# Kernel tuning notes

Measured on AMD Instinct MI355X. Metric: run time of the kernel, lower is better.

Reference implementation:

```python
import jax, jax.numpy as jnp
import numpy as np

N, D, H, E = 50000, 128, 128, 800000


def setup_inputs() -> dict:
    key = jax.random.key(0)
    ks = jax.random.split(key, 12)
    p = lambda k, shape: jax.random.normal(k, shape, dtype=jnp.float32) * 0.02
    z = lambda n: jnp.zeros((n,), jnp.float32)
    return {
        "x1": jax.random.normal(ks[0], (N, D), dtype=jnp.float32),
        "edge_index1": jax.random.randint(ks[1], (2, E), 0, N, dtype=jnp.int32),
        "x2": jax.random.normal(ks[2], (N, D), dtype=jnp.float32),
        "edge_index2": jax.random.randint(ks[3], (2, E), 0, N, dtype=jnp.int32),
        "enc_w1": p(ks[4], (D, H)), "enc_b1": z(H),
        "enc_w2": p(ks[5], (H, H)), "enc_b2": z(H),
        "conv1_w": p(ks[6], (H, H)), "conv1_b": z(H),
        "conv2_w": p(ks[7], (H, H)), "conv2_b": z(H),
        "sim_w1": p(ks[8], (4 * H, H)), "sim_b1": z(H),
        "sim_w2": p(ks[9], (H, 1)), "sim_b2": z(1),
    }


def reference(x1, edge_index1, x2, edge_index2,
              enc_w1, enc_b1, enc_w2, enc_b2,
              conv1_w, conv1_b, conv2_w, conv2_b,
              sim_w1, sim_b1, sim_w2, sim_b2):
    def gcn(x, ei, W, b):
        row, col = ei[0], ei[1]            # [E], [E]
        h = x @ W + b                      # [N, H]
        n = x.shape[0]
        deg = jax.ops.segment_sum(jnp.ones(row.shape[0], h.dtype), row, num_segments=n)
        dis = jnp.where(deg > 0, deg ** -0.5, 0.0)   # deg^-0.5, inf -> 0
        norm = dis[row] * dis[col]         # [E]
        msg = h[col] * norm[:, None]       # gather + per-edge scale, [E, H]
        return jax.ops.segment_sum(msg, row, num_segments=n)  # scatter-add

    def embed(x, ei):
        h = jax.nn.relu(x @ enc_w1 + enc_b1) @ enc_w2 + enc_b2  # encoder MLP
        h = jax.nn.relu(gcn(h, ei, conv1_w, conv1_b))
        h = jax.nn.relu(gcn(h, ei, conv2_w, conv2_b))
        return h.mean(axis=0)              # mean pooling -> [H]

    g1 = embed(x1, edge_index1)
    g2 = embed(x2, edge_index2)
    c = jnp.concatenate([g1, g2, jnp.abs(g1 - g2), g1 * g2], axis=-1)  # [4H]
    return jax.nn.relu(c @ sim_w1 + sim_b1) @ sim_w2 + sim_b2          # [1]
```

## Files before the change

kernel.cpp:

```cpp
#include <hip/hip_runtime.h>
#include <hip/hip_bf16.h>

#define HD 128

typedef short bf16x8 __attribute__((ext_vector_type(8)));
typedef float f32x4 __attribute__((ext_vector_type(4)));

static __device__ inline unsigned short f2b(float f) {
  __hip_bfloat16 h = __float2bfloat16(f);
  return *(unsigned short*)&h;
}
static __device__ inline float b2f(unsigned short u) {
  return __uint_as_float(((unsigned int)u) << 16);
}
static __device__ inline float unpack_lo(unsigned int v) {
  return __uint_as_float(v << 16);
}
static __device__ inline float unpack_hi(unsigned int v) {
  return __uint_as_float(v & 0xffff0000u);
}
static __device__ inline unsigned int pack2(float lo, float hi) {
  return (unsigned int)f2b(lo) | ((unsigned int)f2b(hi) << 16);
}

__global__ void k_deg_slot(const int* __restrict__ ei0, const int* __restrict__ ei1,
                           int E, int N, int* __restrict__ deg2, int* __restrict__ slot) {
  int g = blockIdx.y;
  const int* rows = (g ? ei1 : ei0);
  int base = (blockIdx.x * 256 + threadIdx.x) * 8;
  int* deg = deg2 + g * N;
  int* sl = slot + g * E;
  if (base + 7 < E) {
    int4 r0 = *(const int4*)(rows + base);
    int4 r1 = *(const int4*)(rows + base + 4);
    int4 s0, s1;
    s0.x = atomicAdd(&deg[r0.x], 1);
    s0.y = atomicAdd(&deg[r0.y], 1);
    s0.z = atomicAdd(&deg[r0.z], 1);
    s0.w = atomicAdd(&deg[r0.w], 1);
    s1.x = atomicAdd(&deg[r1.x], 1);
    s1.y = atomicAdd(&deg[r1.y], 1);
    s1.z = atomicAdd(&deg[r1.z], 1);
    s1.w = atomicAdd(&deg[r1.w], 1);
    *(int4*)(sl + base) = s0;
    *(int4*)(sl + base + 4) = s1;
  } else {
    for (int e = base; e < E; ++e) sl[e] = atomicAdd(&deg[rows[e]], 1);
  }
}

__global__ void k_scan_block(const int* __restrict__ deg, int* __restrict__ offs,
                             int* __restrict__ partials, int Ntot) {
  __shared__ int s[256];
  int t = threadIdx.x;
  int i = blockIdx.x * 256 + t;
  int v = (i < Ntot) ? deg[i] : 0;
  s[t] = v;
  __syncthreads();
  #pragma unroll
  for (int off = 1; off < 256; off <<= 1) {
    int x = (t >= off) ? s[t - off] : 0;
    __syncthreads();
    s[t] += x;
    __syncthreads();
  }
  if (i < Ntot) offs[i] = s[t] - v;
  if (t == 255) partials[blockIdx.x] = s[255];
}

__global__ void k_scan_partials(int* __restrict__ partials, int P) {
  __shared__ int s[512];
  int t = threadIdx.x;
  int v = (t < P) ? partials[t] : 0;
  s[t] = v;
  __syncthreads();
  #pragma unroll
  for (int off = 1; off < 512; off <<= 1) {
    int x = (t >= off) ? s[t - off] : 0;
    __syncthreads();
    s[t] += x;
    __syncthreads();
  }
  if (t < P) partials[t] = s[t] - v;
}

__global__ void k_scan_finalize(int* __restrict__ offs, const int* __restrict__ partials,
                                const int* __restrict__ deg, float* __restrict__ dis,
                                int Ntot, int Etot) {
  int i = blockIdx.x * 256 + threadIdx.x;
  if (i < Ntot) {
    offs[i] += partials[blockIdx.x];
    int d = deg[i];
    dis[i] = (d > 0) ? (1.0f / sqrtf((float)d)) : 0.0f;
  }
  if (blockIdx.x == 0 && threadIdx.x == 0) offs[Ntot] = Etot;
}

__global__ void k_csr_fill(const int* __restrict__ ei0, const int* __restrict__ ei1,
                           int E, int N, const int* __restrict__ offs,
                           const int* __restrict__ slot, unsigned short* __restrict__ csr_col) {
  int g = blockIdx.y;
  const int* eg = (g ? ei1 : ei0);
  const int* ob = offs + g * N;
  const int* sl = slot + g * E;
  int base = (blockIdx.x * 256 + threadIdx.x) * 4;
  if (base + 3 < E) {
    int4 r = *(const int4*)(eg + base);
    int4 c = *(const int4*)(eg + E + base);
    int4 s = *(const int4*)(sl + base);
    csr_col[ob[r.x] + s.x] = (unsigned short)c.x;
    csr_col[ob[r.y] + s.y] = (unsigned short)c.y;
    csr_col[ob[r.z] + s.z] = (unsigned short)c.z;
    csr_col[ob[r.w] + s.w] = (unsigned short)c.w;
  } else {
    for (int e = base; e < E; ++e)
      csr_col[ob[eg[e]] + sl[e]] = (unsigned short)eg[E + e];
  }
}

__global__ void k_cvt_w(const float* __restrict__ w0, const float* __restrict__ w1,
                        const float* __restrict__ w2, const float* __restrict__ w3,
                        unsigned short* __restrict__ Wf) {
  int m = blockIdx.x >> 6;
  const float* W = (m == 0) ? w0 : (m == 1) ? w1 : (m == 2) ? w2 : w3;
  int idx = (blockIdx.x & 63) * 256 + threadIdx.x;
  int n = idx & 127, k = idx >> 7;
  float w = W[(size_t)k * HD + n];
  unsigned short h = f2b(w);
  unsigned short l = f2b(w - b2f(h));
  int nt = n >> 4, n16 = n & 15, kc = k >> 5, q = (k >> 3) & 3, j = k & 7;
  int lanei = 16 * q + n16;
  size_t off = ((size_t)(nt * 4 + kc) * 64 + lanei) * 8 + j;
  unsigned short* base = Wf + (size_t)m * 32768;
  base[off] = h;
  base[16384 + off] = l;
}

template<bool RELU, bool SCALE, bool CVT>
__global__ __launch_bounds__(256, 2) void k_gemm_lds(
    const unsigned short* __restrict__ Ab,
    const float* __restrict__ Af0, const float* __restrict__ Af1,
    const unsigned short* __restrict__ Wf, const float* __restrict__ bias,
    const float* __restrict__ scale, unsigned short* __restrict__ C,
    int N, int Ntot) {
  __shared__ unsigned short lds[32768];
  const int tid = threadIdx.x;
  #pragma unroll
  for (int i = 0; i < 16; ++i)
    *(float4*)&lds[(size_t)(i * 256 + tid) * 8] = *(const float4*)&Wf[(size_t)(i * 256 + tid) * 8];
  __syncthreads();

  const int lane = tid & 63;
  const int wave = tid >> 6;
  const int n16 = lane & 15, q = lane >> 4;
  const int rowbase = blockIdx.x * 256 + wave * 64;

  int arow[4];
  #pragma unroll
  for (int t = 0; t < 4; ++t) {
    int r = rowbase + 16 * t + n16;
    arow[t] = (r < Ntot) ? r : (Ntot - 1);
  }

  f32x4 acc[4][8];
  #pragma unroll
  for (int t = 0; t < 4; ++t)
    #pragma unroll
    for (int nt = 0; nt < 8; ++nt) acc[t][nt] = (f32x4){0.f, 0.f, 0.f, 0.f};

  #pragma unroll
  for (int kc = 0; kc < 4; ++kc) {
    bf16x8 a[4];
    #pragma unroll
    for (int t = 0; t < 4; ++t) {
      if (CVT) {
        int r = arow[t];
        const float* src = (r < N) ? (Af0 + (size_t)r * HD) : (Af1 + (size_t)(r - N) * HD);
        float4 u0 = *(const float4*)(src + kc * 32 + q * 8);
        float4 u1 = *(const float4*)(src + kc * 32 + q * 8 + 4);
        union { unsigned short us[8]; bf16x8 v; } tmp;
        tmp.us[0] = f2b(u0.x); tmp.us[1] = f2b(u0.y);
        tmp.us[2] = f2b(u0.z); tmp.us[3] = f2b(u0.w);
        tmp.us[4] = f2b(u1.x); tmp.us[5] = f2b(u1.y);
        tmp.us[6] = f2b(u1.z); tmp.us[7] = f2b(u1.w);
        a[t] = tmp.v;
      } else {
        a[t] = *(const bf16x8*)(Ab + (size_t)arow[t] * HD + kc * 32 + q * 8);
      }
    }
    #pragma unroll
    for (int nt = 0; nt < 8; ++nt) {
      bf16x8 bh = *(const bf16x8*)&lds[(size_t)((nt * 4 + kc) * 64 + lane) * 8];
      bf16x8 bl = *(const bf16x8*)&lds[16384 + (size_t)((nt * 4 + kc) * 64 + lane) * 8];
      #pragma unroll
      for (int t = 0; t < 4; ++t) {
        acc[t][nt] = __builtin_amdgcn_mfma_f32_16x16x32_bf16(a[t], bh, acc[t][nt], 0, 0, 0);
        acc[t][nt] = __builtin_amdgcn_mfma_f32_16x16x32_bf16(a[t], bl, acc[t][nt], 0, 0, 0);
      }
    }
  }

  float bv[8];
  #pragma unroll
  for (int nt = 0; nt < 8; ++nt) bv[nt] = bias[nt * 16 + n16];

  #pragma unroll
  for (int t = 0; t < 4; ++t) {
    #pragma unroll
    for (int r = 0; r < 4; ++r) {
      int row = rowbase + 16 * t + 4 * q + r;
      if (row < Ntot) {
        float s = SCALE ? scale[row] : 1.0f;
        #pragma unroll
        for (int nt = 0; nt < 8; ++nt) {
          float v = acc[t][nt][r] + bv[nt];
          if (RELU) v = fmaxf(v, 0.f);
          if (SCALE) v *= s;
          C[(size_t)row * HD + nt * 16 + n16] = f2b(v);
        }
      }
    }
  }
}

template<bool POOL>
__global__ __launch_bounds__(256) void k_aggregate(
    const unsigned short* __restrict__ T, const int* __restrict__ offs,
    const unsigned short* __restrict__ csr_col, const float* __restrict__ dis,
    unsigned short* __restrict__ out, float* __restrict__ poolrep, int N, int Ntot) {
  __shared__ float red[4][128];
  const int lane = threadIdx.x & 63;
  const int wave = threadIdx.x >> 6;
  const int gw = blockIdx.x * 4 + wave;
  const int sub = lane >> 4, c16 = lane & 15;

  float ax[8];
  #pragma unroll
  for (int j = 0; j < 8; ++j) ax[j] = 0.f;

  if (gw < Ntot) {
    const int beg = offs[gw], end = offs[gw + 1];
    const unsigned int* Tg = (const unsigned int*)T + (size_t)(gw >= N ? N : 0) * 64;
    for (int e = beg; e < end; e += 16) {
      #pragma unroll
      for (int gp = 0; gp < 4; ++gp) {
        if (e + 4 * gp < end) {
          int eg = e + 4 * gp + sub;
          bool valid = (eg < end);
          int ce = valid ? eg : (end - 1);
          int col = csr_col[ce];
          uint4 v = *(const uint4*)(Tg + (size_t)col * 64 + c16 * 4);
          if (!valid) { v.x = 0; v.y = 0; v.z = 0; v.w = 0; }
          ax[0] += unpack_lo(v.x); ax[1] += unpack_hi(v.x);
          ax[2] += unpack_lo(v.y); ax[3] += unpack_hi(v.y);
          ax[4] += unpack_lo(v.z); ax[5] += unpack_hi(v.z);
          ax[6] += unpack_lo(v.w); ax[7] += unpack_hi(v.w);
        }
      }
    }
  }

  #pragma unroll
  for (int j = 0; j < 8; ++j) {
    ax[j] += __shfl_xor(ax[j], 32, 64);
    ax[j] += __shfl_xor(ax[j], 16, 64);
  }
  float dr = (gw < Ntot) ? dis[gw] : 0.f;
  #pragma unroll
  for (int j = 0; j < 8; ++j) ax[j] = fmaxf(ax[j] * dr, 0.f);

  if (!POOL) {
    if (gw < Ntot && sub == 0) {
      uint4 o;
      o.x = pack2(ax[0], ax[1]);
      o.y = pack2(ax[2], ax[3]);
      o.z = pack2(ax[4], ax[5]);
      o.w = pack2(ax[6], ax[7]);
      ((uint4*)out)[(size_t)gw * 16 + c16] = o;
    }
  } else {
    if (sub == 0) {
      *(float4*)&red[wave][c16 * 8]     = make_float4(ax[0], ax[1], ax[2], ax[3]);
      *(float4*)&red[wave][c16 * 8 + 4] = make_float4(ax[4], ax[5], ax[6], ax[7]);
    }
    __syncthreads();
    int t = threadIdx.x;
    if (t < 128) {
      float s = red[0][t] + red[1][t] + red[2][t] + red[3][t];
      int g = (blockIdx.x * 4 >= N) ? 1 : 0;
      atomicAdd(&poolrep[(size_t)((blockIdx.x & 15) * 2 + g) * 128 + t], s);
    }
  }
}

__global__ void k_final(const float* __restrict__ poolrep,
                        const float* __restrict__ W1, const float* __restrict__ b1,
                        const float* __restrict__ W2, const float* __restrict__ b2,
                        float* __restrict__ out, float invN) {
  __shared__ float cs[512];
  __shared__ float red[2];
  int t = threadIdx.x;
  float g1 = 0.f, g2 = 0.f;
  #pragma unroll
  for (int r = 0; r < 16; ++r) {
    g1 += poolrep[r * 256 + t];
    g2 += poolrep[r * 256 + 128 + t];
  }
  g1 *= invN;
  g2 *= invN;
  cs[t] = g1;
  cs[128 + t] = g2;
  cs[256 + t] = fabsf(g1 - g2);
  cs[384 + t] = g1 * g2;
  __syncthreads();
  float acc = b1[t];
  #pragma unroll 8
  for (int i = 0; i < 512; ++i) acc = fmaf(cs[i], W1[(size_t)i * HD + t], acc);
  float h = fmaxf(acc, 0.f);
  float v = h * W2[t];
  #pragma unroll
  for (int off = 32; off > 0; off >>= 1) v += __shfl_down(v, off, 64);
  if ((t & 63) == 0) red[t >> 6] = v;
  __syncthreads();
  if (t == 0) out[0] = red[0] + red[1] + b2[0];
}

extern "C" void kernel_launch(void* const* d_in, const int* in_sizes, int n_in,
                              void* d_out, int out_size, void* d_ws, size_t ws_size,
                              hipStream_t stream) {
  const float* x1     = (const float*)d_in[0];
  const int*   ei1    = (const int*)d_in[1];
  const float* x2     = (const float*)d_in[2];
  const int*   ei2    = (const int*)d_in[3];
  const float* W_in[4] = {(const float*)d_in[4], (const float*)d_in[6],
                          (const float*)d_in[8], (const float*)d_in[10]};
  const float* B_in[4] = {(const float*)d_in[5], (const float*)d_in[7],
                          (const float*)d_in[9], (const float*)d_in[11]};
  const float* sim_w1 = (const float*)d_in[12];
  const float* sim_b1 = (const float*)d_in[13];
  const float* sim_w2 = (const float*)d_in[14];
  const float* sim_b2 = (const float*)d_in[15];

  const int N = in_sizes[0] / HD;
  const int E = in_sizes[1] / 2;
  const int Ntot = 2 * N;

  unsigned short* sp = (unsigned short*)d_ws;
  unsigned short* bufA = sp; sp += (size_t)Ntot * HD;
  unsigned short* bufB = sp; sp += (size_t)Ntot * HD;
  unsigned short* Wf   = sp; sp += 4 * 32768;
  float* fp = (float*)sp;
  float* dis     = fp; fp += Ntot;
  float* poolrep = fp; fp += 16 * 256;
  int* ip = (int*)fp;
  int* deg2     = ip; ip += Ntot;
  int* offs     = ip; ip += Ntot + 1;
  int* partials = ip; ip += 512;
  ip += 1;
  int* slot     = ip; ip += 2 * E;
  unsigned short* csr_col = (unsigned short*)ip;

  const int scanBlocks = (Ntot + 255) / 256;
  const int gemmBlocks = (Ntot + 255) / 256;
  const int aggBlocks  = (Ntot + 3) / 4;
  const dim3 degGrid((E / 8 + 255) / 256, 2);
  const dim3 fillGrid((E / 4 + 255) / 256, 2);

  hipMemsetAsync(poolrep, 0, 16 * 256 * sizeof(float), stream);
  hipMemsetAsync(deg2, 0, (size_t)Ntot * sizeof(int), stream);

  k_cvt_w<<<256, 256, 0, stream>>>(W_in[0], W_in[1], W_in[2], W_in[3], Wf);

  k_deg_slot<<<degGrid, 256, 0, stream>>>(ei1, ei2, E, N, deg2, slot);
  k_scan_block<<<scanBlocks, 256, 0, stream>>>(deg2, offs, partials, Ntot);
  k_scan_partials<<<1, 512, 0, stream>>>(partials, scanBlocks);
  k_scan_finalize<<<scanBlocks, 256, 0, stream>>>(offs, partials, deg2, dis, Ntot, 2 * E);
  k_csr_fill<<<fillGrid, 256, 0, stream>>>(ei1, ei2, E, N, offs, slot, csr_col);

  k_gemm_lds<true,  false, true ><<<gemmBlocks, 256, 0, stream>>>(
      nullptr, x1, x2, Wf + 0 * 32768, B_in[0], nullptr, bufA, N, Ntot);
  k_gemm_lds<false, false, false><<<gemmBlocks, 256, 0, stream>>>(
      bufA, nullptr, nullptr, Wf + 1 * 32768, B_in[1], nullptr, bufB, N, Ntot);
  k_gemm_lds<false, true,  false><<<gemmBlocks, 256, 0, stream>>>(
      bufB, nullptr, nullptr, Wf + 2 * 32768, B_in[2], dis, bufA, N, Ntot);
  k_aggregate<false><<<aggBlocks, 256, 0, stream>>>(bufA, offs, csr_col, dis, bufB, nullptr, N, Ntot);
  k_gemm_lds<false, true,  false><<<gemmBlocks, 256, 0, stream>>>(
      bufB, nullptr, nullptr, Wf + 3 * 32768, B_in[3], dis, bufA, N, Ntot);
  k_aggregate<true ><<<aggBlocks, 256, 0, stream>>>(bufA, offs, csr_col, dis, nullptr, poolrep, N, Ntot);

  k_final<<<1, 128, 0, stream>>>(poolrep, sim_w1, sim_b1, sim_w2, sim_b2,
                                 (float*)d_out, 1.0f / (float)N);
}
```

Measured before the change: 452.3 us.

## Switch activations and weights to fp16 with packed fp16 aggregation

Result: faster. 423.5 us (-6.4%).

```diff
diff --git a/kernel.cpp b/kernel.cpp
--- a/kernel.cpp
+++ b/kernel.cpp
@@ -3,49 +3,34 @@
 
 #define HD 128
 
-typedef short bf16x8 __attribute__((ext_vector_type(8)));
+typedef _Float16 f16x8 __attribute__((ext_vector_type(8)));
+typedef _Float16 f16x2 __attribute__((ext_vector_type(2)));
 typedef float f32x4 __attribute__((ext_vector_type(4)));
 
-static __device__ inline unsigned short f2b(float f) {
-  __hip_bfloat16 h = __float2bfloat16(f);
-  return *(unsigned short*)&h;
-}
-static __device__ inline float b2f(unsigned short u) {
-  return __uint_as_float(((unsigned int)u) << 16);
-}
-static __device__ inline float unpack_lo(unsigned int v) {
-  return __uint_as_float(v << 16);
-}
-static __device__ inline float unpack_hi(unsigned int v) {
-  return __uint_as_float(v & 0xffff0000u);
-}
-static __device__ inline unsigned int pack2(float lo, float hi) {
-  return (unsigned int)f2b(lo) | ((unsigned int)f2b(hi) << 16);
-}
-
 __global__ void k_deg_slot(const int* __restrict__ ei0, const int* __restrict__ ei1,
-                           int E, int N, int* __restrict__ deg2, int* __restrict__ slot) {
+                           int E, int N, int* __restrict__ deg2,
+                           unsigned short* __restrict__ slot) {
   int g = blockIdx.y;
   const int* rows = (g ? ei1 : ei0);
   int base = (blockIdx.x * 256 + threadIdx.x) * 8;
   int* deg = deg2 + g * N;
-  int* sl = slot + g * E;
+  unsigned short* sl = slot + (size_t)g * E;
   if (base + 7 < E) {
     int4 r0 = *(const int4*)(rows + base);
     int4 r1 = *(const int4*)(rows + base + 4);
-    int4 s0, s1;
-    s0.x = atomicAdd(&deg[r0.x], 1);
-    s0.y = atomicAdd(&deg[r0.y], 1);
-    s0.z = atomicAdd(&deg[r0.z], 1);
-    s0.w = atomicAdd(&deg[r0.w], 1);
-    s1.x = atomicAdd(&deg[r1.x], 1);
-    s1.y = atomicAdd(&deg[r1.y], 1);
-    s1.z = atomicAdd(&deg[r1.z], 1);
-    s1.w = atomicAdd(&deg[r1.w], 1);
-    *(int4*)(sl + base) = s0;
-    *(int4*)(sl + base + 4) = s1;
+    union { unsigned short us[8]; uint4 v; } s;
+    s.us[0] = (unsigned short)atomicAdd(&deg[r0.x], 1);
+    s.us[1] = (unsigned short)atomicAdd(&deg[r0.y], 1);
+    s.us[2] = (unsigned short)atomicAdd(&deg[r0.z], 1);
+    s.us[3] = (unsigned short)atomicAdd(&deg[r0.w], 1);
+    s.us[4] = (unsigned short)atomicAdd(&deg[r1.x], 1);
+    s.us[5] = (unsigned short)atomicAdd(&deg[r1.y], 1);
+    s.us[6] = (unsigned short)atomicAdd(&deg[r1.z], 1);
+    s.us[7] = (unsigned short)atomicAdd(&deg[r1.w], 1);
+    *(uint4*)(sl + base) = s.v;
   } else {
-    for (int e = base; e < E; ++e) sl[e] = atomicAdd(&deg[rows[e]], 1);
+    for (int e = base; e < E; ++e)
+      sl[e] = (unsigned short)atomicAdd(&deg[rows[e]], 1);
   }
 }
 
@@ -98,20 +83,21 @@
 
 __global__ void k_csr_fill(const int* __restrict__ ei0, const int* __restrict__ ei1,
                            int E, int N, const int* __restrict__ offs,
-                           const int* __restrict__ slot, unsigned short* __restrict__ csr_col) {
+                           const unsigned short* __restrict__ slot,
+                           unsigned short* __restrict__ csr_col) {
   int g = blockIdx.y;
   const int* eg = (g ? ei1 : ei0);
   const int* ob = offs + g * N;
-  const int* sl = slot + g * E;
+  const unsigned short* sl = slot + (size_t)g * E;
   int base = (blockIdx.x * 256 + threadIdx.x) * 4;
   if (base + 3 < E) {
     int4 r = *(const int4*)(eg + base);
     int4 c = *(const int4*)(eg + E + base);
-    int4 s = *(const int4*)(sl + base);
-    csr_col[ob[r.x] + s.x] = (unsigned short)c.x;
-    csr_col[ob[r.y] + s.y] = (unsigned short)c.y;
-    csr_col[ob[r.z] + s.z] = (unsigned short)c.z;
-    csr_col[ob[r.w] + s.w] = (unsigned short)c.w;
+    uint2 sv = *(const uint2*)(sl + base);
+    csr_col[ob[r.x] + (sv.x & 0xffff)] = (unsigned short)c.x;
+    csr_col[ob[r.y] + (sv.x >> 16)]   = (unsigned short)c.y;
+    csr_col[ob[r.z] + (sv.y & 0xffff)] = (unsigned short)c.z;
+    csr_col[ob[r.w] + (sv.y >> 16)]   = (unsigned short)c.w;
   } else {
     for (int e = base; e < E; ++e)
       csr_col[ob[eg[e]] + sl[e]] = (unsigned short)eg[E + e];
@@ -120,33 +106,29 @@
 
 __global__ void k_cvt_w(const float* __restrict__ w0, const float* __restrict__ w1,
                         const float* __restrict__ w2, const float* __restrict__ w3,
-                        unsigned short* __restrict__ Wf) {
+                        _Float16* __restrict__ Wf) {
   int m = blockIdx.x >> 6;
   const float* W = (m == 0) ? w0 : (m == 1) ? w1 : (m == 2) ? w2 : w3;
   int idx = (blockIdx.x & 63) * 256 + threadIdx.x;
   int n = idx & 127, k = idx >> 7;
   float w = W[(size_t)k * HD + n];
-  unsigned short h = f2b(w);
-  unsigned short l = f2b(w - b2f(h));
   int nt = n >> 4, n16 = n & 15, kc = k >> 5, q = (k >> 3) & 3, j = k & 7;
   int lanei = 16 * q + n16;
   size_t off = ((size_t)(nt * 4 + kc) * 64 + lanei) * 8 + j;
-  unsigned short* base = Wf + (size_t)m * 32768;
-  base[off] = h;
-  base[16384 + off] = l;
+  Wf[(size_t)m * 16384 + off] = (_Float16)w;
 }
 
 template<bool RELU, bool SCALE, bool CVT>
 __global__ __launch_bounds__(256, 2) void k_gemm_lds(
-    const unsigned short* __restrict__ Ab,
+    const _Float16* __restrict__ Ab,
     const float* __restrict__ Af0, const float* __restrict__ Af1,
-    const unsigned short* __restrict__ Wf, const float* __restrict__ bias,
-    const float* __restrict__ scale, unsigned short* __restrict__ C,
+    const _Float16* __restrict__ Wf, const float* __restrict__ bias,
+    const float* __restrict__ scale, _Float16* __restrict__ C,
     int N, int Ntot) {
-  __shared__ unsigned short lds[32768];
+  __shared__ _Float16 lds[16384];
   const int tid = threadIdx.x;
   #pragma unroll
-  for (int i = 0; i < 16; ++i)
+  for (int i = 0; i < 8; ++i)
     *(float4*)&lds[(size_t)(i * 256 + tid) * 8] = *(const float4*)&Wf[(size_t)(i * 256 + tid) * 8];
   __syncthreads();
 
@@ -170,7 +152,7 @@
 
   #pragma unroll
   for (int kc = 0; kc < 4; ++kc) {
-    bf16x8 a[4];
+    f16x8 a[4];
     #pragma unroll
     for (int t = 0; t < 4; ++t) {
       if (CVT) {
@@ -178,25 +160,22 @@
         const float* src = (r < N) ? (Af0 + (size_t)r * HD) : (Af1 + (size_t)(r - N) * HD);
         float4 u0 = *(const float4*)(src + kc * 32 + q * 8);
         float4 u1 = *(const float4*)(src + kc * 32 + q * 8 + 4);
-        union { unsigned short us[8]; bf16x8 v; } tmp;
-        tmp.us[0] = f2b(u0.x); tmp.us[1] = f2b(u0.y);
-        tmp.us[2] = f2b(u0.z); tmp.us[3] = f2b(u0.w);
-        tmp.us[4] = f2b(u1.x); tmp.us[5] = f2b(u1.y);
-        tmp.us[6] = f2b(u1.z); tmp.us[7] = f2b(u1.w);
+        union { _Float16 h[8]; f16x8 v; } tmp;
+        tmp.h[0] = (_Float16)u0.x; tmp.h[1] = (_Float16)u0.y;
+        tmp.h[2] = (_Float16)u0.z; tmp.h[3] = (_Float16)u0.w;
+        tmp.h[4] = (_Float16)u1.x; tmp.h[5] = (_Float16)u1.y;
+        tmp.h[6] = (_Float16)u1.z; tmp.h[7] = (_Float16)u1.w;
         a[t] = tmp.v;
       } else {
-        a[t] = *(const bf16x8*)(Ab + (size_t)arow[t] * HD + kc * 32 + q * 8);
+        a[t] = *(const f16x8*)(Ab + (size_t)arow[t] * HD + kc * 32 + q * 8);
       }
     }
     #pragma unroll
     for (int nt = 0; nt < 8; ++nt) {
-      bf16x8 bh = *(const bf16x8*)&lds[(size_t)((nt * 4 + kc) * 64 + lane) * 8];
-      bf16x8 bl = *(const bf16x8*)&lds[16384 + (size_t)((nt * 4 + kc) * 64 + lane) * 8];
+      f16x8 b = *(const f16x8*)&lds[(size_t)((nt * 4 + kc) * 64 + lane) * 8];
       #pragma unroll
-      for (int t = 0; t < 4; ++t) {
-        acc[t][nt] = __builtin_amdgcn_mfma_f32_16x16x32_bf16(a[t], bh, acc[t][nt], 0, 0, 0);
-        acc[t][nt] = __builtin_amdgcn_mfma_f32_16x16x32_bf16(a[t], bl, acc[t][nt], 0, 0, 0);
-      }
+      for (int t = 0; t < 4; ++t)
+        acc[t][nt] = __builtin_amdgcn_mfma_f32_16x16x32_f16(a[t], b, acc[t][nt], 0, 0, 0);
     }
   }
 
@@ -216,7 +195,7 @@
           float v = acc[t][nt][r] + bv[nt];
           if (RELU) v = fmaxf(v, 0.f);
           if (SCALE) v *= s;
-          C[(size_t)row * HD + nt * 16 + n16] = f2b(v);
+          C[(size_t)row * HD + nt * 16 + n16] = (_Float16)v;
         }
       }
     }
@@ -225,41 +204,54 @@
 
 template<bool POOL>
 __global__ __launch_bounds__(256) void k_aggregate(
-    const unsigned short* __restrict__ T, const int* __restrict__ offs,
+    const _Float16* __restrict__ T, const int* __restrict__ offs,
     const unsigned short* __restrict__ csr_col, const float* __restrict__ dis,
-    unsigned short* __restrict__ out, float* __restrict__ poolrep, int N, int Ntot) {
+    _Float16* __restrict__ out, float* __restrict__ poolrep, int N, int Ntot) {
   __shared__ float red[4][128];
   const int lane = threadIdx.x & 63;
   const int wave = threadIdx.x >> 6;
   const int gw = blockIdx.x * 4 + wave;
   const int sub = lane >> 4, c16 = lane & 15;
 
-  float ax[8];
-  #pragma unroll
-  for (int j = 0; j < 8; ++j) ax[j] = 0.f;
+  f16x2 hacc[4];
+  #pragma unroll
+  for (int j = 0; j < 4; ++j) hacc[j] = (f16x2){(_Float16)0.f, (_Float16)0.f};
 
   if (gw < Ntot) {
     const int beg = offs[gw], end = offs[gw + 1];
-    const unsigned int* Tg = (const unsigned int*)T + (size_t)(gw >= N ? N : 0) * 64;
+    const uint4* Tg = (const uint4*)(T + (size_t)(gw >= N ? N : 0) * HD);
     for (int e = beg; e < end; e += 16) {
+      uint4 v[4];
       #pragma unroll
       for (int gp = 0; gp < 4; ++gp) {
+        v[gp] = make_uint4(0, 0, 0, 0);
         if (e + 4 * gp < end) {
           int eg = e + 4 * gp + sub;
           bool valid = (eg < end);
           int ce = valid ? eg : (end - 1);
           int col = csr_col[ce];
-          uint4 v = *(const uint4*)(Tg + (size_t)col * 64 + c16 * 4);
-          if (!valid) { v.x = 0; v.y = 0; v.z = 0; v.w = 0; }
-          ax[0] += unpack_lo(v.x); ax[1] += unpack_hi(v.x);
-          ax[2] += unpack_lo(v.y); ax[3] += unpack_hi(v.y);
-          ax[4] += unpack_lo(v.z); ax[5] += unpack_hi(v.z);
-          ax[6] += unpack_lo(v.w); ax[7] += unpack_hi(v.w);
+          uint4 t = Tg[(size_t)col * 16 + c16];
+          if (valid) v[gp] = t;
         }
       }
-    }
-  }
-
+      #pragma unroll
+      for (int gp = 0; gp < 4; ++gp) {
+        union { uint4 u; f16x2 h[4]; } w;
+        w.u = v[gp];
+        hacc[0] += w.h[0];
+        hacc[1] += w.h[1];
+        hacc[2] += w.h[2];
+        hacc[3] += w.h[3];
+      }
+    }
+  }
+
+  float ax[8];
+  #pragma unroll
+  for (int j = 0; j < 4; ++j) {
+    ax[2 * j]     = (float)hacc[j][0];
+    ax[2 * j + 1] = (float)hacc[j][1];
+  }
   #pragma unroll
   for (int j = 0; j < 8; ++j) {
     ax[j] += __shfl_xor(ax[j], 32, 64);
@@ -271,12 +263,10 @@
 
   if (!POOL) {
     if (gw < Ntot && sub == 0) {
-      uint4 o;
-      o.x = pack2(ax[0], ax[1]);
-      o.y = pack2(ax[2], ax[3]);
-      o.z = pack2(ax[4], ax[5]);
-      o.w = pack2(ax[6], ax[7]);
-      ((uint4*)out)[(size_t)gw * 16 + c16] = o;
+      union { uint4 u; _Float16 h[8]; } o;
+      #pragma unroll
+      for (int j = 0; j < 8; ++j) o.h[j] = (_Float16)ax[j];
+      ((uint4*)out)[(size_t)gw * 16 + c16] = o.u;
     }
   } else {
     if (sub == 0) {
@@ -345,10 +335,10 @@
   const int E = in_sizes[1] / 2;
   const int Ntot = 2 * N;
 
-  unsigned short* sp = (unsigned short*)d_ws;
-  unsigned short* bufA = sp; sp += (size_t)Ntot * HD;
-  unsigned short* bufB = sp; sp += (size_t)Ntot * HD;
-  unsigned short* Wf   = sp; sp += 4 * 32768;
+  _Float16* sp = (_Float16*)d_ws;
+  _Float16* bufA = sp; sp += (size_t)Ntot * HD;
+  _Float16* bufB = sp; sp += (size_t)Ntot * HD;
+  _Float16* Wf   = sp; sp += 4 * 16384;
   float* fp = (float*)sp;
   float* dis     = fp; fp += Ntot;
   float* poolrep = fp; fp += 16 * 256;
@@ -356,9 +346,9 @@
   int* deg2     = ip; ip += Ntot;
   int* offs     = ip; ip += Ntot + 1;
   int* partials = ip; ip += 512;
-  ip += 1;
-  int* slot     = ip; ip += 2 * E;
-  unsigned short* csr_col = (unsigned short*)ip;
+  ip = (int*)(((uintptr_t)ip + 15) & ~(uintptr_t)15);
+  unsigned short* slot = (unsigned short*)ip;
+  unsigned short* csr_col = slot + 2 * (size_t)E;
 
   const int scanBlocks = (Ntot + 255) / 256;
   const int gemmBlocks = (Ntot + 255) / 256;
@@ -366,8 +356,7 @@
   const dim3 degGrid((E / 8 + 255) / 256, 2);
   const dim3 fillGrid((E / 4 + 255) / 256, 2);
 
-  hipMemsetAsync(poolrep, 0, 16 * 256 * sizeof(float), stream);
-  hipMemsetAsync(deg2, 0, (size_t)Ntot * sizeof(int), stream);
+  hipMemsetAsync(poolrep, 0, (16 * 256 + Ntot) * sizeof(float), stream);
 
   k_cvt_w<<<256, 256, 0, stream>>>(W_in[0], W_in[1], W_in[2], W_in[3], Wf);
 
@@ -378,14 +367,14 @@
   k_csr_fill<<<fillGrid, 256, 0, stream>>>(ei1, ei2, E, N, offs, slot, csr_col);
 
   k_gemm_lds<true,  false, true ><<<gemmBlocks, 256, 0, stream>>>(
-      nullptr, x1, x2, Wf + 0 * 32768, B_in[0], nullptr, bufA, N, Ntot);
+      nullptr, x1, x2, Wf + 0 * 16384, B_in[0], nullptr, bufA, N, Ntot);
   k_gemm_lds<false, false, false><<<gemmBlocks, 256, 0, stream>>>(
-      bufA, nullptr, nullptr, Wf + 1 * 32768, B_in[1], nullptr, bufB, N, Ntot);
+      bufA, nullptr, nullptr, Wf + 1 * 16384, B_in[1], nullptr, bufB, N, Ntot);
   k_gemm_lds<false, true,  false><<<gemmBlocks, 256, 0, stream>>>(
-      bufB, nullptr, nullptr, Wf + 2 * 32768, B_in[2], dis, bufA, N, Ntot);
+      bufB, nullptr, nullptr, Wf + 2 * 16384, B_in[2], dis, bufA, N, Ntot);
   k_aggregate<false><<<aggBlocks, 256, 0, stream>>>(bufA, offs, csr_col, dis, bufB, nullptr, N, Ntot);
   k_gemm_lds<false, true,  false><<<gemmBlocks, 256, 0, stream>>>(
-      bufB, nullptr, nullptr, Wf + 3 * 32768, B_in[3], dis, bufA, N, Ntot);
+      bufB, nullptr, nullptr, Wf + 3 * 16384, B_in[3], dis, bufA, N, Ntot);
   k_aggregate<true ><<<aggBlocks, 256, 0, stream>>>(bufA, offs, csr_col, dis, nullptr, poolrep, N, Ntot);
 
   k_final<<<1, 128, 0, stream>>>(poolrep, sim_w1, sim_b1, sim_w2, sim_b2,
```
